# Performance work log

Hardware: AMD Instinct MI355X
Metric: run time of the kernel (lower is better)

Reference implementation:

```python
import jax, jax.numpy as jnp
import numpy as np

N = 100000
E = 1600000
IN_C = 128
HID = 32
OUT_C = 32
HEADS = 4
NEG_SLOPE = 0.2


def setup_inputs() -> dict:
    key = jax.random.key(0)
    ks = jax.random.split(key, 8)
    x = jax.random.normal(ks[0], (N, IN_C), dtype=jnp.float32)
    edge_index = jax.random.randint(ks[1], (2, E), 0, N, dtype=jnp.int64)
    s = 0.1
    W1 = jax.random.normal(ks[2], (IN_C, HEADS * HID), dtype=jnp.float32) * s
    att_src1 = jax.random.normal(ks[3], (HEADS, HID), dtype=jnp.float32) * s
    att_dst1 = jax.random.normal(ks[4], (HEADS, HID), dtype=jnp.float32) * s
    W2 = jax.random.normal(ks[5], (HEADS * HID, HEADS * OUT_C), dtype=jnp.float32) * s
    att_src2 = jax.random.normal(ks[6], (HEADS, OUT_C), dtype=jnp.float32) * s
    att_dst2 = jax.random.normal(ks[7], (HEADS, OUT_C), dtype=jnp.float32) * s
    return {"x": x, "edge_index": edge_index, "W1": W1, "att_src1": att_src1,
            "att_dst1": att_dst1, "W2": W2, "att_src2": att_src2, "att_dst2": att_dst2}


def _gat_conv(x, src, dst, W, a_src, a_dst, heads, ch):
    # linear transform: [N, heads, ch]
    h = (x @ W).reshape(-1, heads, ch)
    # per-node attention logits [N, heads]
    al_src = jnp.sum(h * a_src, axis=-1)
    al_dst = jnp.sum(h * a_dst, axis=-1)
    # per-edge attention [E, heads]
    e = jax.nn.leaky_relu(al_src[src] + al_dst[dst], negative_slope=NEG_SLOPE)
    # segment softmax over incoming edges of each dst node
    m = jax.ops.segment_max(e, dst, num_segments=N)
    e = jnp.exp(e - m[dst])
    denom = jax.ops.segment_sum(e, dst, num_segments=N)
    alpha = e / (denom[dst] + 1e-16)
    # message + scatter-add aggregation
    msg = h[src] * alpha[:, :, None]          # [E, heads, ch]
    out = jax.ops.segment_sum(msg, dst, num_segments=N)
    return out.reshape(-1, heads * ch)        # concat heads (PyG default)


def reference(x, edge_index, W1, att_src1, att_dst1, W2, att_src2, att_dst2):
    # add self-loops (PyG GATConv default add_self_loops=True)
    loop = jnp.arange(N, dtype=edge_index.dtype)
    src = jnp.concatenate([edge_index[0], loop])
    dst = jnp.concatenate([edge_index[1], loop])
    h = _gat_conv(x, src, dst, W1, att_src1, att_dst1, HEADS, HID)
    h = jax.nn.relu(h)  # dropout is identity in eval mode
    out = _gat_conv(h, src, dst, W2, att_src2, att_dst2, HEADS, OUT_C)
    return out
```

## Files before the change

kernel.cpp:

```cpp
#include <hip/hip_runtime.h>

#define NN 100000
#define EE 1600000
#define NGRP 8
#define DRANGE 12500
#define SLOTS 72
#define NROWPAD 100032
#define NTILES 1563

#define PX_BLK 1024
#define PW_BLK 32
#define WA_BLK 16
#define PREP_BLK (PX_BLK + PW_BLK + WA_BLK)
#define BUILD_BLK 1568

typedef short bf16x8 __attribute__((ext_vector_type(8)));
typedef float f32x4 __attribute__((ext_vector_type(4)));

__device__ __forceinline__ float leaky(float x) { return x > 0.f ? x : 0.2f * x; }

__device__ __forceinline__ unsigned int bfpack2(float a, float b)
{
    unsigned int xa = __float_as_uint(a), xb = __float_as_uint(b);
    xa = (xa + 0x7fffu + ((xa >> 16) & 1u)) >> 16;
    xb = (xb + 0x7fffu + ((xb >> 16) & 1u)) & 0xffff0000u;
    return xa | xb;
}

__device__ __forceinline__ unsigned short bf1(float a)
{
    unsigned int x = __float_as_uint(a);
    return (unsigned short)((x + 0x7fffu + ((x >> 16) & 1u)) >> 16);
}

__device__ __forceinline__ float blo(unsigned int u) { return __uint_as_float(u << 16); }
__device__ __forceinline__ float bhi(unsigned int u) { return __uint_as_float(u & 0xffff0000u); }


__global__ __launch_bounds__(256) void prep_build(const float* __restrict__ X,
                                                  unsigned int* __restrict__ Xbf,
                                                  const float* __restrict__ W1, const float* __restrict__ W2,
                                                  unsigned short* __restrict__ Wtb1, unsigned short* __restrict__ Wtb2,
                                                  const float* __restrict__ as1, const float* __restrict__ ad1,
                                                  const float* __restrict__ as2, const float* __restrict__ ad2,
                                                  unsigned short* __restrict__ Wa1, unsigned short* __restrict__ Wa2,
                                                  const int* __restrict__ src, const int* __restrict__ dst,
                                                  int* __restrict__ cnt, int* __restrict__ csr)
{
    const int bid = blockIdx.x;
    if (bid < PX_BLK) {
        const int tid0 = bid * 256 + threadIdx.x;
        const int nthr = PX_BLK * 256;
        const int total = NROWPAD * 16;
        for (int i = tid0; i < total; i += nthr) {
            int row = i >> 4, inner = i & 15;
            uint4 o;
            if (row < NN) {
                const float* p = X + (size_t)row * 128 + inner * 8;
                float4 f0 = *(const float4*)p;
                float4 f1 = *(const float4*)(p + 4);
                o.x = bfpack2(f0.x, f0.y); o.y = bfpack2(f0.z, f0.w);
                o.z = bfpack2(f1.x, f1.y); o.w = bfpack2(f1.z, f1.w);
            } else {
                o = make_uint4(0, 0, 0, 0);
            }
            *(uint4*)&Xbf[(size_t)i * 4] = o;
        }
    } else if (bid < PX_BLK + PW_BLK) {
        int tid = (bid - PX_BLK) * 256 + threadIdx.x;
        int layer = tid >> 12;
        int rem = tid & 4095;
        int c = rem >> 5;
        int kq = (rem & 31) * 4;
        const float* Ws = layer ? W2 : W1;
        unsigned short* Wd = layer ? Wtb2 : Wtb1;
        ushort4 o;
        o.x = bf1(Ws[(kq + 0) * 128 + c]);
        o.y = bf1(Ws[(kq + 1) * 128 + c]);
        o.z = bf1(Ws[(kq + 2) * 128 + c]);
        o.w = bf1(Ws[(kq + 3) * 128 + c]);
        *(ushort4*)&Wd[c * 128 + kq] = o;
    } else if (bid < PREP_BLK) {
        int tid = (bid - PX_BLK - PW_BLK) * 256 + threadIdx.x;
        int layer = tid >> 11;
        int rem = tid & 2047;
        int col = rem >> 7;
        int k = rem & 127;
        const float* Ws = layer ? W2 : W1;
        unsigned short* Wd = layer ? Wa2 : Wa1;
        float s = 0.f;
        if (col < 8) {
            int head = col & 3;
            const float* av = (col < 4) ? (layer ? as2 : as1) : (layer ? ad2 : ad1);
            const float* wr = Ws + k * 128 + head * 32;
            const float* ar = av + head * 32;
            #pragma unroll
            for (int c = 0; c < 32; c++) s += wr[c] * ar[c];
        }
        Wd[col * 128 + k] = bf1(s);
    } else {
        const int bb = bid - PREP_BLK;
        const int grp = bb & (NGRP - 1);
        const int gr  = bb >> 3;
        const int ng  = BUILD_BLK >> 3;
        const int dlo = grp * DRANGE, dhi = dlo + DRANGE;
        const int tid0 = gr * 256 + threadIdx.x;
        const int nthr = ng * 256;
        for (int e4 = tid0 * 4; e4 < EE; e4 += nthr * 4) {
            int4 dv = *(const int4*)&dst[e4];
            int4 sv = *(const int4*)&src[e4];
            #pragma unroll
            for (int j = 0; j < 4; ++j) {
                int d = (&dv.x)[j];
                if (d >= dlo && d < dhi) {
                    int pos = atomicAdd(&cnt[d], 1);
                    if (pos < SLOTS) csr[(size_t)d * SLOTS + pos] = (&sv.x)[j];
                }
            }
        }
    }
}


__global__ __launch_bounds__(256) void gemm_mfma(const unsigned short* __restrict__ Xbf,
                                                 const unsigned short* __restrict__ Wtb,
                                                 const unsigned short* __restrict__ Wa,
                                                 unsigned int* __restrict__ Hbf,
                                                 float* __restrict__ alS, float* __restrict__ alD)
{
    const int w = threadIdx.x >> 6, lane = threadIdx.x & 63;
    const int cl = lane & 15, b = lane >> 4;

    bf16x8 Bf[8][4];
    #pragma unroll
    for (int c = 0; c < 8; c++)
        #pragma unroll
        for (int s = 0; s < 4; s++)
            Bf[c][s] = *(const bf16x8*)(Wtb + (16 * c + cl) * 128 + 32 * s + 8 * b);

    bf16x8 Bf9[4];
    #pragma unroll
    for (int s = 0; s < 4; s++)
        Bf9[s] = *(const bf16x8*)(Wa + cl * 128 + 32 * s + 8 * b);

    for (int tile = blockIdx.x; tile < NTILES; tile += gridDim.x) {
        const int rowb = tile * 64 + 16 * w;
        const unsigned short* pa = Xbf + (size_t)(rowb + cl) * 128 + 8 * b;
        bf16x8 Af[4];
        #pragma unroll
        for (int s = 0; s < 4; s++) Af[s] = *(const bf16x8*)(pa + 32 * s);

        f32x4 acc[8];
        #pragma unroll
        for (int c = 0; c < 8; c++) acc[c] = (f32x4){0.f, 0.f, 0.f, 0.f};
        f32x4 acc9 = (f32x4){0.f, 0.f, 0.f, 0.f};
        #pragma unroll
        for (int s = 0; s < 4; s++) {
            #pragma unroll
            for (int c = 0; c < 8; c++)
                acc[c] = __builtin_amdgcn_mfma_f32_16x16x32_bf16(Af[s], Bf[c][s], acc[c], 0, 0, 0);
            acc9 = __builtin_amdgcn_mfma_f32_16x16x32_bf16(Af[s], Bf9[s], acc9, 0, 0, 0);
        }

        const int row0 = rowb + 4 * b;
        #pragma unroll
        for (int c = 0; c < 8; c++) {
            #pragma unroll
            for (int r = 0; r < 4; r++) {
                float partner = __shfl_xor(acc[c][r], 1);
                if (!(cl & 1) && row0 + r < NN)
                    Hbf[(size_t)(row0 + r) * 64 + 8 * c + (cl >> 1)] = bfpack2(acc[c][r], partner);
            }
        }
        #pragma unroll
        for (int r = 0; r < 4; r++) {
            const int rr = row0 + r;
            if (rr < NN) {
                if (cl < 4)      alS[rr * 4 + cl] = acc9[r];
                else if (cl < 8) alD[rr * 4 + (cl - 4)] = acc9[r];
            }
        }
    }
}


__global__ __launch_bounds__(256) void agg_kernel(const unsigned int* __restrict__ Hbf,
                                                  const int* __restrict__ cnt, const int* __restrict__ csr,
                                                  const float* __restrict__ alS, const float* __restrict__ alD,
                                                  float* __restrict__ OUTf, unsigned int* __restrict__ OUTb,
                                                  int do_relu)
{
    __shared__ float pl[4][64 * 4];
    __shared__ int   sl[4][64];
    const int w = threadIdx.x >> 6, lane = threadIdx.x & 63;
    const int wid = (blockIdx.x * 256 + threadIdx.x) >> 6;
    if (wid >= NN) return;
    const int nreal = min(cnt[wid], SLOTS);
    const int nE = nreal + 1;
    const float4 ad = *(const float4*)&alD[wid * 4];
    const int half = lane >> 5, l5 = lane & 31;
    const int hq = l5 >> 3;
    const uint2* __restrict__ H2 = (const uint2*)Hbf + l5;
    const int* __restrict__ slots = csr + (size_t)wid * SLOTS;

    float4 acc = make_float4(0.f, 0.f, 0.f, 0.f);
    float den = 0.f;
    for (int base = 0; base < nE; base += 64) {
        const int nthis = min(64, nE - base);
        const int idx = base + lane;
        int s_ = 0;
        float4 p = make_float4(0.f, 0.f, 0.f, 0.f);
        if (lane < nthis) {
            s_ = (idx == nreal) ? wid : slots[idx];
            float4 as = *(const float4*)&alS[s_ * 4];
            p.x = __expf(leaky(as.x + ad.x));
            p.y = __expf(leaky(as.y + ad.y));
            p.z = __expf(leaky(as.z + ad.z));
            p.w = __expf(leaky(as.w + ad.w));
        }
        sl[w][lane] = s_;
        *(float4*)&pl[w][lane * 4] = p;
        int k = 0;
        for (; k + 8 <= nthis; k += 8) {
            float p0 = pl[w][(k + half) * 4 + hq];
            float p1 = pl[w][(k + 2 + half) * 4 + hq];
            float p2 = pl[w][(k + 4 + half) * 4 + hq];
            float p3 = pl[w][(k + 6 + half) * 4 + hq];
            int s0i = sl[w][k + half];
            int s1i = sl[w][k + 2 + half];
            int s2i = sl[w][k + 4 + half];
            int s3i = sl[w][k + 6 + half];
            uint2 u0 = H2[(size_t)s0i * 32];
            uint2 u1 = H2[(size_t)s1i * 32];
            uint2 u2 = H2[(size_t)s2i * 32];
            uint2 u3 = H2[(size_t)s3i * 32];
            den += (p0 + p1) + (p2 + p3);
            acc.x += p0 * blo(u0.x); acc.y += p0 * bhi(u0.x);
            acc.z += p0 * blo(u0.y); acc.w += p0 * bhi(u0.y);
            acc.x += p1 * blo(u1.x); acc.y += p1 * bhi(u1.x);
            acc.z += p1 * blo(u1.y); acc.w += p1 * bhi(u1.y);
            acc.x += p2 * blo(u2.x); acc.y += p2 * bhi(u2.x);
            acc.z += p2 * blo(u2.y); acc.w += p2 * bhi(u2.y);
            acc.x += p3 * blo(u3.x); acc.y += p3 * bhi(u3.x);
            acc.z += p3 * blo(u3.y); acc.w += p3 * bhi(u3.y);
        }
        for (; k < nthis; k += 2) {
            float paf = pl[w][(k + half) * 4 + hq];
            int sa = sl[w][k + half];
            uint2 ua = H2[(size_t)sa * 32];
            den += paf;
            acc.x += paf * blo(ua.x); acc.y += paf * bhi(ua.x);
            acc.z += paf * blo(ua.y); acc.w += paf * bhi(ua.y);
        }
    }
    acc.x += __shfl_xor(acc.x, 32);
    acc.y += __shfl_xor(acc.y, 32);
    acc.z += __shfl_xor(acc.z, 32);
    acc.w += __shfl_xor(acc.w, 32);
    den   += __shfl_xor(den,   32);
    if (half == 0) {
        float inv = 1.f / (den + 1e-16f);
        float o0 = acc.x * inv, o1 = acc.y * inv, o2 = acc.z * inv, o3 = acc.w * inv;
        if (do_relu) {
            o0 = fmaxf(o0, 0.f); o1 = fmaxf(o1, 0.f);
            o2 = fmaxf(o2, 0.f); o3 = fmaxf(o3, 0.f);
        }
        if (OUTb) {
            uint2 ov;
            ov.x = bfpack2(o0, o1);
            ov.y = bfpack2(o2, o3);
            *(uint2*)&OUTb[(size_t)wid * 64 + l5 * 2] = ov;
        } else {
            *(float4*)&OUTf[(size_t)wid * 128 + l5 * 4] = make_float4(o0, o1, o2, o3);
        }
    }
}


extern "C" void kernel_launch(void* const* d_in, const int* in_sizes, int n_in,
                              void* d_out, int out_size, void* d_ws, size_t ws_size,
                              hipStream_t stream)
{
    const float* x   = (const float*)d_in[0];
    const int*   ei  = (const int*)d_in[1];
    const float* W1  = (const float*)d_in[2];
    const float* as1 = (const float*)d_in[3];
    const float* ad1 = (const float*)d_in[4];
    const float* W2  = (const float*)d_in[5];
    const float* as2 = (const float*)d_in[6];
    const float* ad2 = (const float*)d_in[7];
    const int* srcp = ei;
    const int* dstp = ei + EE;

    char* w = (char*)d_ws;
    unsigned int* Xbf  = (unsigned int*)w; w += (size_t)NROWPAD * 64 * 4;
    unsigned int* Hbf  = (unsigned int*)w; w += (size_t)NN * 64 * 4;
    unsigned short* Wtb1 = (unsigned short*)w; w += 16384 * 2;
    unsigned short* Wtb2 = (unsigned short*)w; w += 16384 * 2;
    unsigned short* Wa1  = (unsigned short*)w; w += 2048 * 2;
    unsigned short* Wa2  = (unsigned short*)w; w += 2048 * 2;
    float* alS = (float*)w; w += (size_t)NN * 4 * 4;
    float* alD = (float*)w; w += (size_t)NN * 4 * 4;
    int* cnt    = (int*)w;  w += (size_t)NN * 4;
    int* csr    = (int*)w;  w += (size_t)NN * SLOTS * 4;

    hipMemsetAsync(cnt, 0, NN * sizeof(int), stream);
    prep_build<<<PREP_BLK + BUILD_BLK, 256, 0, stream>>>(x, Xbf, W1, W2, Wtb1, Wtb2,
                                                         as1, ad1, as2, ad2, Wa1, Wa2,
                                                         srcp, dstp, cnt, csr);

    const int node_wave_blocks = (NN + 3) / 4;

    gemm_mfma<<<512, 256, 0, stream>>>((const unsigned short*)Xbf, Wtb1, Wa1, Hbf, alS, alD);
    agg_kernel<<<node_wave_blocks, 256, 0, stream>>>(Hbf, cnt, csr, alS, alD, nullptr, Xbf, 1);

    gemm_mfma<<<512, 256, 0, stream>>>((const unsigned short*)Xbf, Wtb2, Wa2, Hbf, alS, alD);
    agg_kernel<<<node_wave_blocks, 256, 0, stream>>>(Hbf, cnt, csr, alS, alD, (float*)d_out, nullptr, 0);
}
```

Measured before the change: 284.2 us.

## Fuse fp32-to-bf16 conversion into layer-1 GEMM and split CSR build kernel

Drops the separate pass that converts X to bf16 and instead converts fp32 rows inside the first MFMA GEMM, saving one full read and write of X. The CSR build moves out of the combined prep kernel into its own flat kernel: each thread takes four edges, with no eight-way destination-range partitioning and no repeated scans of the edge list. The hipMemset is replaced by zeroing cnt inside the prep kernel, and nontemporal loads and stores are added in the aggregation kernel. The build now runs after prep instead of overlapping with it, and its atomics are spread across all nodes at once, which may hurt locality.

```diff
diff --git a/kernel.cpp b/kernel.cpp
--- a/kernel.cpp
+++ b/kernel.cpp
@@ -2,20 +2,14 @@
 
 #define NN 100000
 #define EE 1600000
-#define NGRP 8
-#define DRANGE 12500
 #define SLOTS 72
 #define NROWPAD 100032
 #define NTILES 1563
 
-#define PX_BLK 1024
-#define PW_BLK 32
-#define WA_BLK 16
-#define PREP_BLK (PX_BLK + PW_BLK + WA_BLK)
-#define BUILD_BLK 1568
-
 typedef short bf16x8 __attribute__((ext_vector_type(8)));
 typedef float f32x4 __attribute__((ext_vector_type(4)));
+typedef int   i32x4 __attribute__((ext_vector_type(4)));
+typedef unsigned int u32x2 __attribute__((ext_vector_type(2)));
 
 __device__ __forceinline__ float leaky(float x) { return x > 0.f ? x : 0.2f * x; }
 
@@ -37,37 +31,16 @@
 __device__ __forceinline__ float bhi(unsigned int u) { return __uint_as_float(u & 0xffff0000u); }
 
 
-__global__ __launch_bounds__(256) void prep_build(const float* __restrict__ X,
-                                                  unsigned int* __restrict__ Xbf,
-                                                  const float* __restrict__ W1, const float* __restrict__ W2,
-                                                  unsigned short* __restrict__ Wtb1, unsigned short* __restrict__ Wtb2,
-                                                  const float* __restrict__ as1, const float* __restrict__ ad1,
-                                                  const float* __restrict__ as2, const float* __restrict__ ad2,
-                                                  unsigned short* __restrict__ Wa1, unsigned short* __restrict__ Wa2,
-                                                  const int* __restrict__ src, const int* __restrict__ dst,
-                                                  int* __restrict__ cnt, int* __restrict__ csr)
+__global__ __launch_bounds__(256) void prep_kernel(const float* __restrict__ W1, const float* __restrict__ W2,
+                                                   unsigned short* __restrict__ Wtb1, unsigned short* __restrict__ Wtb2,
+                                                   const float* __restrict__ as1, const float* __restrict__ ad1,
+                                                   const float* __restrict__ as2, const float* __restrict__ ad2,
+                                                   unsigned short* __restrict__ Wa1, unsigned short* __restrict__ Wa2,
+                                                   unsigned int* __restrict__ Xbf, int* __restrict__ cnt)
 {
     const int bid = blockIdx.x;
-    if (bid < PX_BLK) {
-        const int tid0 = bid * 256 + threadIdx.x;
-        const int nthr = PX_BLK * 256;
-        const int total = NROWPAD * 16;
-        for (int i = tid0; i < total; i += nthr) {
-            int row = i >> 4, inner = i & 15;
-            uint4 o;
-            if (row < NN) {
-                const float* p = X + (size_t)row * 128 + inner * 8;
-                float4 f0 = *(const float4*)p;
-                float4 f1 = *(const float4*)(p + 4);
-                o.x = bfpack2(f0.x, f0.y); o.y = bfpack2(f0.z, f0.w);
-                o.z = bfpack2(f1.x, f1.y); o.w = bfpack2(f1.z, f1.w);
-            } else {
-                o = make_uint4(0, 0, 0, 0);
-            }
-            *(uint4*)&Xbf[(size_t)i * 4] = o;
-        }
-    } else if (bid < PX_BLK + PW_BLK) {
-        int tid = (bid - PX_BLK) * 256 + threadIdx.x;
+    if (bid < 32) {
+        int tid = bid * 256 + threadIdx.x;
         int layer = tid >> 12;
         int rem = tid & 4095;
         int c = rem >> 5;
@@ -80,8 +53,8 @@
         o.z = bf1(Ws[(kq + 2) * 128 + c]);
         o.w = bf1(Ws[(kq + 3) * 128 + c]);
         *(ushort4*)&Wd[c * 128 + kq] = o;
-    } else if (bid < PREP_BLK) {
-        int tid = (bid - PX_BLK - PW_BLK) * 256 + threadIdx.x;
+    } else if (bid < 48) {
+        int tid = (bid - 32) * 256 + threadIdx.x;
         int layer = tid >> 11;
         int rem = tid & 2047;
         int col = rem >> 7;
@@ -98,31 +71,35 @@
             for (int c = 0; c < 32; c++) s += wr[c] * ar[c];
         }
         Wd[col * 128 + k] = bf1(s);
+    } else if (bid < 148) {
+        int t = (bid - 48) * 256 + threadIdx.x;
+        if (t < 25000) ((i32x4*)cnt)[t] = (i32x4){0, 0, 0, 0};
     } else {
-        const int bb = bid - PREP_BLK;
-        const int grp = bb & (NGRP - 1);
-        const int gr  = bb >> 3;
-        const int ng  = BUILD_BLK >> 3;
-        const int dlo = grp * DRANGE, dhi = dlo + DRANGE;
-        const int tid0 = gr * 256 + threadIdx.x;
-        const int nthr = ng * 256;
-        for (int e4 = tid0 * 4; e4 < EE; e4 += nthr * 4) {
-            int4 dv = *(const int4*)&dst[e4];
-            int4 sv = *(const int4*)&src[e4];
-            #pragma unroll
-            for (int j = 0; j < 4; ++j) {
-                int d = (&dv.x)[j];
-                if (d >= dlo && d < dhi) {
-                    int pos = atomicAdd(&cnt[d], 1);
-                    if (pos < SLOTS) csr[(size_t)d * SLOTS + pos] = (&sv.x)[j];
-                }
-            }
-        }
-    }
-}
-
-
-__global__ __launch_bounds__(256) void gemm_mfma(const unsigned short* __restrict__ Xbf,
+        int t = (bid - 148) * 256 + threadIdx.x;
+        ((uint4*)Xbf)[NN * 16 + t] = make_uint4(0, 0, 0, 0);
+    }
+}
+
+
+__global__ __launch_bounds__(256) void build_kernel(const int* __restrict__ src, const int* __restrict__ dst,
+                                                    int* __restrict__ cnt, int* __restrict__ csr)
+{
+    const int t = blockIdx.x * 256 + threadIdx.x;
+    if (t >= EE / 4) return;
+    const int e4 = t * 4;
+    i32x4 dv = __builtin_nontemporal_load((const i32x4*)(dst + e4));
+    i32x4 sv = __builtin_nontemporal_load((const i32x4*)(src + e4));
+    #pragma unroll
+    for (int j = 0; j < 4; ++j) {
+        int d = dv[j];
+        int pos = atomicAdd(&cnt[d], 1);
+        if (pos < SLOTS) atomicExch(&csr[(size_t)d * SLOTS + pos], sv[j]);
+    }
+}
+
+
+template<bool FP32IN>
+__global__ __launch_bounds__(256) void gemm_mfma(const void* __restrict__ Xin,
                                                  const unsigned short* __restrict__ Wtb,
                                                  const unsigned short* __restrict__ Wa,
                                                  unsigned int* __restrict__ Hbf,
@@ -145,10 +122,31 @@
 
     for (int tile = blockIdx.x; tile < NTILES; tile += gridDim.x) {
         const int rowb = tile * 64 + 16 * w;
-        const unsigned short* pa = Xbf + (size_t)(rowb + cl) * 128 + 8 * b;
+        const int rA = rowb + cl;
         bf16x8 Af[4];
-        #pragma unroll
-        for (int s = 0; s < 4; s++) Af[s] = *(const bf16x8*)(pa + 32 * s);
+        if constexpr (FP32IN) {
+            if (rA < NN) {
+                const float* pa = (const float*)Xin + (size_t)rA * 128 + 8 * b;
+                #pragma unroll
+                for (int s = 0; s < 4; s++) {
+                    float4 f0 = *(const float4*)(pa + 32 * s);
+                    float4 f1 = *(const float4*)(pa + 32 * s + 4);
+                    union { bf16x8 v; unsigned int u[4]; } cv;
+                    cv.u[0] = bfpack2(f0.x, f0.y); cv.u[1] = bfpack2(f0.z, f0.w);
+                    cv.u[2] = bfpack2(f1.x, f1.y); cv.u[3] = bfpack2(f1.z, f1.w);
+                    Af[s] = cv.v;
+                }
+            } else {
+                union { bf16x8 v; unsigned int u[4]; } cz;
+                cz.u[0] = cz.u[1] = cz.u[2] = cz.u[3] = 0;
+                #pragma unroll
+                for (int s = 0; s < 4; s++) Af[s] = cz.v;
+            }
+        } else {
+            const unsigned short* pa = (const unsigned short*)Xin + (size_t)rA * 128 + 8 * b;
+            #pragma unroll
+            for (int s = 0; s < 4; s++) Af[s] = *(const bf16x8*)(pa + 32 * s);
+        }
 
         f32x4 acc[8];
         #pragma unroll
@@ -211,7 +209,7 @@
         int s_ = 0;
         float4 p = make_float4(0.f, 0.f, 0.f, 0.f);
         if (lane < nthis) {
-            s_ = (idx == nreal) ? wid : slots[idx];
+            s_ = (idx == nreal) ? wid : __builtin_nontemporal_load(slots + idx);
             float4 as = *(const float4*)&alS[s_ * 4];
             p.x = __expf(leaky(as.x + ad.x));
             p.y = __expf(leaky(as.y + ad.y));
@@ -266,12 +264,11 @@
             o2 = fmaxf(o2, 0.f); o3 = fmaxf(o3, 0.f);
         }
         if (OUTb) {
-            uint2 ov;
-            ov.x = bfpack2(o0, o1);
-            ov.y = bfpack2(o2, o3);
-            *(uint2*)&OUTb[(size_t)wid * 64 + l5 * 2] = ov;
+            u32x2 ov = { bfpack2(o0, o1), bfpack2(o2, o3) };
+            __builtin_nontemporal_store(ov, (u32x2*)&OUTb[(size_t)wid * 64 + l5 * 2]);
         } else {
-            *(float4*)&OUTf[(size_t)wid * 128 + l5 * 4] = make_float4(o0, o1, o2, o3);
+            f32x4 ov = { o0, o1, o2, o3 };
+            __builtin_nontemporal_store(ov, (f32x4*)&OUTf[(size_t)wid * 128 + l5 * 4]);
         }
     }
 }
@@ -304,16 +301,15 @@
     int* cnt    = (int*)w;  w += (size_t)NN * 4;
     int* csr    = (int*)w;  w += (size_t)NN * SLOTS * 4;
 
-    hipMemsetAsync(cnt, 0, NN * sizeof(int), stream);
-    prep_build<<<PREP_BLK + BUILD_BLK, 256, 0, stream>>>(x, Xbf, W1, W2, Wtb1, Wtb2,
-                                                         as1, ad1, as2, ad2, Wa1, Wa2,
-                                                         srcp, dstp, cnt, csr);
+    prep_kernel<<<150, 256, 0, stream>>>(W1, W2, Wtb1, Wtb2, as1, ad1, as2, ad2, Wa1, Wa2,
+                                         Xbf, cnt);
+    build_kernel<<<(EE / 4 + 255) / 256, 256, 0, stream>>>(srcp, dstp, cnt, csr);
 
     const int node_wave_blocks = (NN + 3) / 4;
 
-    gemm_mfma<<<512, 256, 0, stream>>>((const unsigned short*)Xbf, Wtb1, Wa1, Hbf, alS, alD);
+    gemm_mfma<true><<<512, 256, 0, stream>>>(x, Wtb1, Wa1, Hbf, alS, alD);
     agg_kernel<<<node_wave_blocks, 256, 0, stream>>>(Hbf, cnt, csr, alS, alD, nullptr, Xbf, 1);
 
-    gemm_mfma<<<512, 256, 0, stream>>>((const unsigned short*)Xbf, Wtb2, Wa2, Hbf, alS, alD);
+    gemm_mfma<false><<<512, 256, 0, stream>>>(Xbf, Wtb2, Wa2, Hbf, alS, alD);
     agg_kernel<<<node_wave_blocks, 256, 0, stream>>>(Hbf, cnt, csr, alS, alD, (float*)d_out, nullptr, 0);
 }
```

After: 363.6 us. +27.9%, slower.
